# Optimization experiments

Hardware: AMD Instinct MI355X
Metric: run time of the kernel (lower is better)

Reference implementation:

```python
import jax, jax.numpy as jnp
import numpy as np

E, U, D, R = 200000, 50000, 128, 32
N2, N1, NU = 100000, 80000, 20000  # hop-2 frontier, hop-1 frontier, unreachable; N1+N2+NU == E
M1, M0 = 1600000, 800000


def setup_inputs() -> dict:
    key = jax.random.key(0)
    ks = jax.random.split(key, 16)
    inp = {
        'ent_emb': jax.random.normal(ks[0], (E, D), jnp.float32) * 0.1,
        'user_emb': jax.random.normal(ks[1], (U, D), jnp.float32) * 0.1,
        'rel_emb': jax.random.normal(ks[2], (R, D), jnp.float32) * 0.1,
        'W_self': jax.random.normal(ks[3], (D, D), jnp.float32) / np.sqrt(D),
        'W_nei': jax.random.normal(ks[4], (D, D), jnp.float32) / np.sqrt(D),
        'b': jnp.zeros((D,), jnp.float32),
        'final_indices': jax.random.randint(ks[5], (N2,), 0, E, jnp.int32),
        'ent_now1': jax.random.randint(ks[6], (N1,), 0, E, jnp.int32),
        'e1_src': jax.random.randint(ks[7], (M1,), 0, N2, jnp.int32),
        'e1_dst': jax.random.randint(ks[8], (M1,), 0, N1, jnp.int32),
        'e1_rel': jax.random.randint(ks[9], (M1,), 0, R, jnp.int32),
        'e0_src': jax.random.randint(ks[10], (M0,), 0, N1, jnp.int32),
        'e0_dst': jax.random.randint(ks[11], (M0,), 0, U, jnp.int32),
        'e0_rel': jax.random.randint(ks[12], (M0,), 0, R, jnp.int32),
        'unreach_idx': jax.random.randint(ks[13], (NU,), 0, E, jnp.int32),
        'order': jax.random.permutation(ks[14], E).astype(jnp.int32),
    }
    return inp


def _rgcn_layer(x, tail, src, dst, rel, W_self, W_nei, b, rel_emb, n_out, activate):
    # self transform: [N, D]
    out = x @ W_self + b
    if tail is not None:
        # gather neighbor reps + relation modulation: [M, D]
        msg = tail[src] * rel_emb[rel]
        agg = jax.ops.segment_sum(msg, dst, num_segments=n_out)
        deg = jax.ops.segment_sum(jnp.ones_like(dst, dtype=x.dtype), dst, num_segments=n_out)
        agg = agg / jnp.clip(deg, 1.0)[:, None]
        out = out + agg @ W_nei
    return jnp.tanh(out) if activate else out


def reference(ent_emb, user_emb, rel_emb, W_self, W_nei, b,
              final_indices, ent_now1, e1_src, e1_dst, e1_rel,
              e0_src, e0_dst, e0_rel, unreach_idx, order):
    # hop 2: raw gathered entity embeddings (deepest frontier)
    h2 = ent_emb[final_indices]                                            # [N2, D]
    # hop 1: RGCN over kg edges from hop-2 frontier
    h1 = _rgcn_layer(ent_emb[ent_now1], h2, e1_src, e1_dst, e1_rel,
                     W_self, W_nei, b, rel_emb, N1, activate=True)          # [N1, D]
    # hop 0: user representations, no activation (activate=False in source)
    user_rep = _rgcn_layer(user_emb, h1, e0_src, e0_dst, e0_rel,
                           W_self, W_nei, b, rel_emb, U, activate=False)    # [U, D]
    # unreachable entities: self-only transform (tail_rep=None)
    unreachable = _rgcn_layer(ent_emb[unreach_idx], None, None, None, None,
                              W_self, W_nei, b, rel_emb, NU, activate=True)  # [NU, D]
    # concat hop reps in forward hop order, then reindex-scatter by entity order
    ent_user_all = jnp.concatenate([h1, h2, unreachable], axis=0)[order]    # [E, D]
    return jnp.concatenate([user_rep, ent_user_all], axis=0)               # [U+E, D]
```

## Files before the change

### kernel.cpp

```cpp
#include <hip/hip_runtime.h>

#define E_  200000
#define U_  50000
#define D_  128
#define R_  32
#define N2_ 100000
#define N1_ 80000
#define NU_ 20000
#define M1_ 1600000
#define M0_ 800000

__device__ __forceinline__ float4 ld4(const float* p) {
    return *reinterpret_cast<const float4*>(p);
}
__device__ __forceinline__ void st4(float* p, float4 v) {
    *reinterpret_cast<float4*>(p) = v;
}

__device__ __forceinline__ float fast_tanh(float x) {
    float e = __expf(2.0f * x);
    return 1.0f - 2.0f / (e + 1.0f);
}

__global__ __launch_bounds__(256) void gather_rows_k(
    const float* __restrict__ src, const int* __restrict__ idx,
    float* __restrict__ out, int n)
{
    long long gid = (long long)blockIdx.x * blockDim.x + threadIdx.x;
    int i = (int)(gid >> 5);
    int l = (int)(gid & 31);
    if (i >= n) return;
    int s = idx[i];
    st4(out + (long long)i * 128 + l * 4, ld4(src + (long long)s * 128 + l * 4));
}

__global__ __launch_bounds__(256) void hist_k(
    const int* __restrict__ dst, int* __restrict__ cnt, int M)
{
    int i = blockIdx.x * blockDim.x + threadIdx.x;
    if (i < M) atomicAdd(&cnt[dst[i]], 1);
}

__global__ __launch_bounds__(1024) void scan_k(
    int* __restrict__ cur, int* __restrict__ off, int N)
{
    __shared__ int ls[1024];
    const int t = threadIdx.x;
    const int chunk = (N + 1023) >> 10;
    const int s = t * chunk;
    const int e = min(s + chunk, N);
    int sum = 0;
    for (int i = s; i < e; ++i) sum += cur[i];
    ls[t] = sum;
    __syncthreads();
    #pragma unroll
    for (int d = 1; d < 1024; d <<= 1) {
        int v = (t >= d) ? ls[t - d] : 0;
        __syncthreads();
        ls[t] += v;
        __syncthreads();
    }
    int run = (t == 0) ? 0 : ls[t - 1];
    for (int i = s; i < e; ++i) {
        int c = cur[i];
        off[i] = run;
        cur[i] = run;
        run += c;
    }
    if (t == 1023) off[N] = ls[1023];
}

__global__ __launch_bounds__(256) void fill_k(
    const int* __restrict__ src, const int* __restrict__ dst,
    const int* __restrict__ rel, int* __restrict__ cur,
    int* __restrict__ sorted, int M)
{
    int i = blockIdx.x * blockDim.x + threadIdx.x;
    if (i >= M) return;
    int p = atomicAdd(&cur[dst[i]], 1);
    sorted[p] = src[i] | (rel[i] << 20);
}

__global__ __launch_bounds__(256) void seg_reduce_k(
    const float* __restrict__ tail, const float* __restrict__ rel_emb,
    const int* __restrict__ off, const int* __restrict__ sorted,
    float* __restrict__ aggout, int N)
{
    long long gid = (long long)blockIdx.x * blockDim.x + threadIdx.x;
    int row = (int)(gid >> 5);
    int l = (int)(gid & 31) * 4;
    if (row >= N) return;
    int s = off[row], e = off[row + 1];
    float4 acc = make_float4(0.f, 0.f, 0.f, 0.f);
    int j = s;
    for (; j + 1 < e; j += 2) {
        int p0 = sorted[j], p1 = sorted[j + 1];
        float4 t0 = ld4(tail + (long long)(p0 & 0xFFFFF) * 128 + l);
        float4 r0 = ld4(rel_emb + (long long)(p0 >> 20) * 128 + l);
        float4 t1 = ld4(tail + (long long)(p1 & 0xFFFFF) * 128 + l);
        float4 r1 = ld4(rel_emb + (long long)(p1 >> 20) * 128 + l);
        acc.x = fmaf(t0.x, r0.x, acc.x); acc.y = fmaf(t0.y, r0.y, acc.y);
        acc.z = fmaf(t0.z, r0.z, acc.z); acc.w = fmaf(t0.w, r0.w, acc.w);
        acc.x = fmaf(t1.x, r1.x, acc.x); acc.y = fmaf(t1.y, r1.y, acc.y);
        acc.z = fmaf(t1.z, r1.z, acc.z); acc.w = fmaf(t1.w, r1.w, acc.w);
    }
    if (j < e) {
        int p0 = sorted[j];
        float4 t0 = ld4(tail + (long long)(p0 & 0xFFFFF) * 128 + l);
        float4 r0 = ld4(rel_emb + (long long)(p0 >> 20) * 128 + l);
        acc.x = fmaf(t0.x, r0.x, acc.x); acc.y = fmaf(t0.y, r0.y, acc.y);
        acc.z = fmaf(t0.z, r0.z, acc.z); acc.w = fmaf(t0.w, r0.w, acc.w);
    }
    float sc = 1.0f / (float)max(e - s, 1);
    acc.x *= sc; acc.y *= sc; acc.z *= sc; acc.w *= sc;
    st4(aggout + (long long)row * 128 + l, acc);
}

template<bool GATHER, bool ACCUM, bool BIAS, bool ACT>
__global__ __launch_bounds__(256) void gemm_rows_k(
    const float* __restrict__ X, const int* __restrict__ idx,
    const float* __restrict__ W, const float* __restrict__ bias,
    float* __restrict__ Out, int N)
{
    __shared__ float XsT[32][128];
    __shared__ float Ws [32][128];
    const int tid = threadIdx.x;
    const int rowbase = blockIdx.x * 128;
    const int rg = tid >> 4;
    const int cg = tid & 15;
    const int r0 = rg * 8;
    const int c0 = cg * 8;

    float acc[8][8];
    if (BIAS) {
        #pragma unroll
        for (int j = 0; j < 8; ++j) {
            float bv = bias[c0 + j];
            #pragma unroll
            for (int i = 0; i < 8; ++i) acc[i][j] = bv;
        }
    } else {
        #pragma unroll
        for (int i = 0; i < 8; ++i)
            #pragma unroll
            for (int j = 0; j < 8; ++j) acc[i][j] = 0.0f;
    }

    const int srow = tid >> 3;
    const int skq  = (tid & 7) * 4;
    const int sswz = (tid & 7) << 2;
    const int wkk  = tid >> 5;
    const int wcc  = (tid & 31) * 4;

    for (int k0 = 0; k0 < 128; k0 += 32) {
        __syncthreads();
        #pragma unroll
        for (int p = 0; p < 4; ++p) {
            int row = p * 32 + srow;
            int grow = rowbase + row;
            int cl = grow < N ? grow : (N - 1);
            const float* xr;
            if (GATHER) xr = X + (long long)idx[cl] * 128;
            else        xr = X + (long long)cl * 128;
            float4 v = ld4(xr + k0 + skq);
            int rs = row ^ sswz;
            XsT[skq + 0][rs] = v.x;
            XsT[skq + 1][rs] = v.y;
            XsT[skq + 2][rs] = v.z;
            XsT[skq + 3][rs] = v.w;
        }
        #pragma unroll
        for (int p = 0; p < 4; ++p) {
            int k = p * 8 + wkk;
            st4(&Ws[k][wcc], ld4(W + (long long)(k0 + k) * 128 + wcc));
        }
        __syncthreads();
        #pragma unroll
        for (int k = 0; k < 32; ++k) {
            int A0 = (((r0 >> 2) ^ ((k >> 2) & 7)) << 2);
            float4 x0 = ld4(&XsT[k][A0]);
            float4 x1 = ld4(&XsT[k][A0 ^ 4]);
            float4 w0 = ld4(&Ws[k][c0]);
            float4 w1 = ld4(&Ws[k][c0 + 4]);
            float xs[8] = {x0.x, x0.y, x0.z, x0.w, x1.x, x1.y, x1.z, x1.w};
            float ws[8] = {w0.x, w0.y, w0.z, w0.w, w1.x, w1.y, w1.z, w1.w};
            #pragma unroll
            for (int i = 0; i < 8; ++i)
                #pragma unroll
                for (int j = 0; j < 8; ++j)
                    acc[i][j] = fmaf(xs[i], ws[j], acc[i][j]);
        }
    }

    #pragma unroll
    for (int i = 0; i < 8; ++i) {
        int row = rowbase + r0 + i;
        if (row >= N) continue;
        float* op = Out + (long long)row * 128 + c0;
        float vals[8];
        #pragma unroll
        for (int j = 0; j < 8; ++j) vals[j] = acc[i][j];
        if (ACCUM) {
            float4 o0 = ld4(op), o1 = ld4(op + 4);
            vals[0] += o0.x; vals[1] += o0.y; vals[2] += o0.z; vals[3] += o0.w;
            vals[4] += o1.x; vals[5] += o1.y; vals[6] += o1.z; vals[7] += o1.w;
        }
        if (ACT) {
            #pragma unroll
            for (int j = 0; j < 8; ++j) vals[j] = fast_tanh(vals[j]);
        }
        st4(op,     make_float4(vals[0], vals[1], vals[2], vals[3]));
        st4(op + 4, make_float4(vals[4], vals[5], vals[6], vals[7]));
    }
}

extern "C" void kernel_launch(void* const* d_in, const int* in_sizes, int n_in,
                              void* d_out, int out_size, void* d_ws, size_t ws_size,
                              hipStream_t stream)
{
    const float* ent_emb  = (const float*)d_in[0];
    const float* user_emb = (const float*)d_in[1];
    const float* rel_emb  = (const float*)d_in[2];
    const float* W_self   = (const float*)d_in[3];
    const float* W_nei    = (const float*)d_in[4];
    const float* bvec     = (const float*)d_in[5];
    const int* final_indices = (const int*)d_in[6];
    const int* ent_now1   = (const int*)d_in[7];
    const int* e1_src     = (const int*)d_in[8];
    const int* e1_dst     = (const int*)d_in[9];
    const int* e1_rel     = (const int*)d_in[10];
    const int* e0_src     = (const int*)d_in[11];
    const int* e0_dst     = (const int*)d_in[12];
    const int* e0_rel     = (const int*)d_in[13];
    const int* unreach_idx = (const int*)d_in[14];
    const int* order      = (const int*)d_in[15];

    float* out = (float*)d_out;
    float* ws  = (float*)d_ws;

    float* concat = ws;
    float* agg1 = concat + (size_t)E_ * 128;
    float* agg0 = agg1 + (size_t)N1_ * 128;
    int* cur1 = (int*)(agg0 + (size_t)U_ * 128);
    int* cur0 = cur1 + N1_;
    int* off1 = cur0 + U_;
    int* off0 = off1 + (N1_ + 1);
    int* sorted1 = off0 + (U_ + 1);
    int* sorted0 = sorted1 + M1_;

    float* h1   = concat;
    float* h2   = concat + (size_t)N1_ * 128;
    float* unre = concat + (size_t)(N1_ + N2_) * 128;

    hipMemsetAsync(cur1, 0, (size_t)(N1_ + U_) * sizeof(int), stream);

    gather_rows_k<<<(N2_ * 32 + 255) / 256, 256, 0, stream>>>(
        ent_emb, final_indices, h2, N2_);

    hist_k<<<(M1_ + 255) / 256, 256, 0, stream>>>(e1_dst, cur1, M1_);
    scan_k<<<1, 1024, 0, stream>>>(cur1, off1, N1_);
    fill_k<<<(M1_ + 255) / 256, 256, 0, stream>>>(
        e1_src, e1_dst, e1_rel, cur1, sorted1, M1_);
    seg_reduce_k<<<(N1_ * 32 + 255) / 256, 256, 0, stream>>>(
        h2, rel_emb, off1, sorted1, agg1, N1_);

    gemm_rows_k<true,  false, true,  false><<<(N1_ + 127) / 128, 256, 0, stream>>>(
        ent_emb, ent_now1, W_self, bvec, h1, N1_);
    gemm_rows_k<false, true,  false, true ><<<(N1_ + 127) / 128, 256, 0, stream>>>(
        agg1, nullptr, W_nei, nullptr, h1, N1_);

    hist_k<<<(M0_ + 255) / 256, 256, 0, stream>>>(e0_dst, cur0, M0_);
    scan_k<<<1, 1024, 0, stream>>>(cur0, off0, U_);
    fill_k<<<(M0_ + 255) / 256, 256, 0, stream>>>(
        e0_src, e0_dst, e0_rel, cur0, sorted0, M0_);
    seg_reduce_k<<<(U_ * 32 + 255) / 256, 256, 0, stream>>>(
        h1, rel_emb, off0, sorted0, agg0, U_);

    gemm_rows_k<false, false, true,  false><<<(U_ + 127) / 128, 256, 0, stream>>>(
        user_emb, nullptr, W_self, bvec, out, U_);
    gemm_rows_k<false, true,  false, false><<<(U_ + 127) / 128, 256, 0, stream>>>(
        agg0, nullptr, W_nei, nullptr, out, U_);

    gemm_rows_k<true,  false, true,  true ><<<(NU_ + 127) / 128, 256, 0, stream>>>(
        ent_emb, unreach_idx, W_self, bvec, unre, NU_);

    gather_rows_k<<<(E_ * 32 + 255) / 256, 256, 0, stream>>>(
        concat, order, out + (size_t)U_ * 128, E_);
}
```

Baseline: 1.136 ms.

## Parallelize degree prefix scan and fuse self/neighbor GEMMs into one kernel

The single-block serial scan over per-destination counts becomes a three-kernel multi-block scan: block partial sums, a scan over the partials, then per-block apply. The paired self-transform and neighbor-transform GEMMs (run as a write followed by an accumulate pass) are merged into one kernel that stages both inputs and both weight tiles and accumulates into a single register tile. This avoids re-reading and re-writing the output between passes. It doubles shared memory per block (64KB), which may cut occupancy.

```diff
diff --git a/kernel.cpp b/kernel.cpp
--- a/kernel.cpp
+++ b/kernel.cpp
@@ -41,33 +41,83 @@
     if (i < M) atomicAdd(&cnt[dst[i]], 1);
 }
 
-__global__ __launch_bounds__(1024) void scan_k(
-    int* __restrict__ cur, int* __restrict__ off, int N)
-{
-    __shared__ int ls[1024];
+__global__ __launch_bounds__(256) void partial_sums_k(
+    const int* __restrict__ cnt, int* __restrict__ bsum, int N)
+{
+    __shared__ int sm[256];
     const int t = threadIdx.x;
-    const int chunk = (N + 1023) >> 10;
-    const int s = t * chunk;
-    const int e = min(s + chunk, N);
+    const int base = blockIdx.x * 1024;
     int sum = 0;
-    for (int i = s; i < e; ++i) sum += cur[i];
-    ls[t] = sum;
+    #pragma unroll
+    for (int i = 0; i < 4; ++i) {
+        int g = base + t + i * 256;
+        if (g < N) sum += cnt[g];
+    }
+    sm[t] = sum;
     __syncthreads();
     #pragma unroll
-    for (int d = 1; d < 1024; d <<= 1) {
-        int v = (t >= d) ? ls[t - d] : 0;
-        __syncthreads();
-        ls[t] += v;
-        __syncthreads();
-    }
-    int run = (t == 0) ? 0 : ls[t - 1];
-    for (int i = s; i < e; ++i) {
-        int c = cur[i];
-        off[i] = run;
-        cur[i] = run;
-        run += c;
-    }
-    if (t == 1023) off[N] = ls[1023];
+    for (int s = 128; s > 0; s >>= 1) {
+        if (t < s) sm[t] += sm[t + s];
+        __syncthreads();
+    }
+    if (t == 0) bsum[blockIdx.x] = sm[0];
+}
+
+__global__ __launch_bounds__(256) void scan_partials_k(
+    int* __restrict__ bsum, int NB, int* __restrict__ off, int N)
+{
+    __shared__ int ls[256];
+    const int t = threadIdx.x;
+    int v = (t < NB) ? bsum[t] : 0;
+    ls[t] = v;
+    __syncthreads();
+    #pragma unroll
+    for (int d = 1; d < 256; d <<= 1) {
+        int u = (t >= d) ? ls[t - d] : 0;
+        __syncthreads();
+        ls[t] += u;
+        __syncthreads();
+    }
+    if (t < NB) bsum[t] = ls[t] - v;
+    if (t == 255) off[N] = ls[255];
+}
+
+__global__ __launch_bounds__(256) void scan_apply_k(
+    const int* __restrict__ cnt, const int* __restrict__ bsum,
+    int* __restrict__ off, int* __restrict__ cur, int N)
+{
+    __shared__ int buf[1024];
+    __shared__ int ts[256];
+    const int t = threadIdx.x;
+    const int base = blockIdx.x * 1024;
+    #pragma unroll
+    for (int i = 0; i < 4; ++i) {
+        int g = base + t + i * 256;
+        buf[t + i * 256] = (g < N) ? cnt[g] : 0;
+    }
+    __syncthreads();
+    const int a = buf[t * 4], b = buf[t * 4 + 1], c = buf[t * 4 + 2], d = buf[t * 4 + 3];
+    const int s = a + b + c + d;
+    ts[t] = s;
+    __syncthreads();
+    #pragma unroll
+    for (int dd = 1; dd < 256; dd <<= 1) {
+        int u = (t >= dd) ? ts[t - dd] : 0;
+        __syncthreads();
+        ts[t] += u;
+        __syncthreads();
+    }
+    const int pre = bsum[blockIdx.x] + ts[t] - s;
+    const int o0 = pre, o1 = pre + a, o2 = o1 + b, o3 = o2 + c;
+    const int g0 = base + t * 4;
+    if (g0 + 3 < N) {
+        *reinterpret_cast<int4*>(off + g0) = make_int4(o0, o1, o2, o3);
+        *reinterpret_cast<int4*>(cur + g0) = make_int4(o0, o1, o2, o3);
+    } else {
+        if (g0     < N) { off[g0]     = o0; cur[g0]     = o0; }
+        if (g0 + 1 < N) { off[g0 + 1] = o1; cur[g0 + 1] = o1; }
+        if (g0 + 2 < N) { off[g0 + 2] = o2; cur[g0 + 2] = o2; }
+    }
 }
 
 __global__ __launch_bounds__(256) void fill_k(
@@ -126,10 +176,8 @@
     __shared__ float Ws [32][128];
     const int tid = threadIdx.x;
     const int rowbase = blockIdx.x * 128;
-    const int rg = tid >> 4;
-    const int cg = tid & 15;
-    const int r0 = rg * 8;
-    const int c0 = cg * 8;
+    const int r0 = (tid >> 4) * 8;
+    const int c0 = (tid & 15) * 8;
 
     float acc[8][8];
     if (BIAS) {
@@ -159,9 +207,8 @@
             int row = p * 32 + srow;
             int grow = rowbase + row;
             int cl = grow < N ? grow : (N - 1);
-            const float* xr;
-            if (GATHER) xr = X + (long long)idx[cl] * 128;
-            else        xr = X + (long long)cl * 128;
+            const float* xr = GATHER ? X + (long long)idx[cl] * 128
+                                     : X + (long long)cl * 128;
             float4 v = ld4(xr + k0 + skq);
             int rs = row ^ sswz;
             XsT[skq + 0][rs] = v.x;
@@ -205,6 +252,103 @@
             vals[0] += o0.x; vals[1] += o0.y; vals[2] += o0.z; vals[3] += o0.w;
             vals[4] += o1.x; vals[5] += o1.y; vals[6] += o1.z; vals[7] += o1.w;
         }
+        if (ACT) {
+            #pragma unroll
+            for (int j = 0; j < 8; ++j) vals[j] = fast_tanh(vals[j]);
+        }
+        st4(op,     make_float4(vals[0], vals[1], vals[2], vals[3]));
+        st4(op + 4, make_float4(vals[4], vals[5], vals[6], vals[7]));
+    }
+}
+
+template<bool GATHER1, bool ACT>
+__global__ __launch_bounds__(256) void gemm_fused_k(
+    const float* __restrict__ X1, const int* __restrict__ idx,
+    const float* __restrict__ X2,
+    const float* __restrict__ W1, const float* __restrict__ W2,
+    const float* __restrict__ bias, float* __restrict__ Out, int N)
+{
+    __shared__ float X1sT[32][128];
+    __shared__ float X2sT[32][128];
+    __shared__ float W1s [32][128];
+    __shared__ float W2s [32][128];
+    const int tid = threadIdx.x;
+    const int rowbase = blockIdx.x * 128;
+    const int r0 = (tid >> 4) * 8;
+    const int c0 = (tid & 15) * 8;
+
+    float acc[8][8];
+    #pragma unroll
+    for (int j = 0; j < 8; ++j) {
+        float bv = bias[c0 + j];
+        #pragma unroll
+        for (int i = 0; i < 8; ++i) acc[i][j] = bv;
+    }
+
+    const int srow = tid >> 3;
+    const int skq  = (tid & 7) * 4;
+    const int sswz = (tid & 7) << 2;
+    const int wkk  = tid >> 5;
+    const int wcc  = (tid & 31) * 4;
+
+    for (int k0 = 0; k0 < 128; k0 += 32) {
+        __syncthreads();
+        #pragma unroll
+        for (int p = 0; p < 4; ++p) {
+            int row = p * 32 + srow;
+            int grow = rowbase + row;
+            int cl = grow < N ? grow : (N - 1);
+            const float* x1r = GATHER1 ? X1 + (long long)idx[cl] * 128
+                                       : X1 + (long long)cl * 128;
+            const float* x2r = X2 + (long long)cl * 128;
+            float4 v1 = ld4(x1r + k0 + skq);
+            float4 v2 = ld4(x2r + k0 + skq);
+            int rs = row ^ sswz;
+            X1sT[skq + 0][rs] = v1.x; X1sT[skq + 1][rs] = v1.y;
+            X1sT[skq + 2][rs] = v1.z; X1sT[skq + 3][rs] = v1.w;
+            X2sT[skq + 0][rs] = v2.x; X2sT[skq + 1][rs] = v2.y;
+            X2sT[skq + 2][rs] = v2.z; X2sT[skq + 3][rs] = v2.w;
+        }
+        #pragma unroll
+        for (int p = 0; p < 4; ++p) {
+            int k = p * 8 + wkk;
+            st4(&W1s[k][wcc], ld4(W1 + (long long)(k0 + k) * 128 + wcc));
+            st4(&W2s[k][wcc], ld4(W2 + (long long)(k0 + k) * 128 + wcc));
+        }
+        __syncthreads();
+        #pragma unroll
+        for (int k = 0; k < 32; ++k) {
+            int A0 = (((r0 >> 2) ^ ((k >> 2) & 7)) << 2);
+            float4 a0 = ld4(&X1sT[k][A0]);
+            float4 a1 = ld4(&X1sT[k][A0 ^ 4]);
+            float4 b0 = ld4(&X2sT[k][A0]);
+            float4 b1 = ld4(&X2sT[k][A0 ^ 4]);
+            float4 u0 = ld4(&W1s[k][c0]);
+            float4 u1 = ld4(&W1s[k][c0 + 4]);
+            float4 v0 = ld4(&W2s[k][c0]);
+            float4 v1 = ld4(&W2s[k][c0 + 4]);
+            float x1s[8] = {a0.x, a0.y, a0.z, a0.w, a1.x, a1.y, a1.z, a1.w};
+            float x2s[8] = {b0.x, b0.y, b0.z, b0.w, b1.x, b1.y, b1.z, b1.w};
+            float w1s[8] = {u0.x, u0.y, u0.z, u0.w, u1.x, u1.y, u1.z, u1.w};
+            float w2s[8] = {v0.x, v0.y, v0.z, v0.w, v1.x, v1.y, v1.z, v1.w};
+            #pragma unroll
+            for (int i = 0; i < 8; ++i)
+                #pragma unroll
+                for (int j = 0; j < 8; ++j) {
+                    acc[i][j] = fmaf(x1s[i], w1s[j], acc[i][j]);
+                    acc[i][j] = fmaf(x2s[i], w2s[j], acc[i][j]);
+                }
+        }
+    }
+
+    #pragma unroll
+    for (int i = 0; i < 8; ++i) {
+        int row = rowbase + r0 + i;
+        if (row >= N) continue;
+        float* op = Out + (long long)row * 128 + c0;
+        float vals[8];
+        #pragma unroll
+        for (int j = 0; j < 8; ++j) vals[j] = acc[i][j];
         if (ACT) {
             #pragma unroll
             for (int j = 0; j < 8; ++j) vals[j] = fast_tanh(vals[j]);
@@ -244,44 +388,49 @@
     int* cur1 = (int*)(agg0 + (size_t)U_ * 128);
     int* cur0 = cur1 + N1_;
     int* off1 = cur0 + U_;
-    int* off0 = off1 + (N1_ + 1);
-    int* sorted1 = off0 + (U_ + 1);
+    int* off0 = off1 + (N1_ + 4);
+    int* bsum1 = off0 + (U_ + 4);
+    int* bsum0 = bsum1 + 256;
+    int* sorted1 = bsum0 + 256;
     int* sorted0 = sorted1 + M1_;
 
     float* h1   = concat;
     float* h2   = concat + (size_t)N1_ * 128;
     float* unre = concat + (size_t)(N1_ + N2_) * 128;
 
+    const int NB1 = (N1_ + 1023) / 1024;
+    const int NB0 = (U_  + 1023) / 1024;
+
     hipMemsetAsync(cur1, 0, (size_t)(N1_ + U_) * sizeof(int), stream);
 
     gather_rows_k<<<(N2_ * 32 + 255) / 256, 256, 0, stream>>>(
         ent_emb, final_indices, h2, N2_);
 
     hist_k<<<(M1_ + 255) / 256, 256, 0, stream>>>(e1_dst, cur1, M1_);
-    scan_k<<<1, 1024, 0, stream>>>(cur1, off1, N1_);
+    partial_sums_k<<<NB1, 256, 0, stream>>>(cur1, bsum1, N1_);
+    scan_partials_k<<<1, 256, 0, stream>>>(bsum1, NB1, off1, N1_);
+    scan_apply_k<<<NB1, 256, 0, stream>>>(cur1, bsum1, off1, cur1, N1_);
     fill_k<<<(M1_ + 255) / 256, 256, 0, stream>>>(
         e1_src, e1_dst, e1_rel, cur1, sorted1, M1_);
     seg_reduce_k<<<(N1_ * 32 + 255) / 256, 256, 0, stream>>>(
         h2, rel_emb, off1, sorted1, agg1, N1_);
 
-    gemm_rows_k<true,  false, true,  false><<<(N1_ + 127) / 128, 256, 0, stream>>>(
-        ent_emb, ent_now1, W_self, bvec, h1, N1_);
-    gemm_rows_k<false, true,  false, true ><<<(N1_ + 127) / 128, 256, 0, stream>>>(
-        agg1, nullptr, W_nei, nullptr, h1, N1_);
+    gemm_fused_k<true, true><<<(N1_ + 127) / 128, 256, 0, stream>>>(
+        ent_emb, ent_now1, agg1, W_self, W_nei, bvec, h1, N1_);
 
     hist_k<<<(M0_ + 255) / 256, 256, 0, stream>>>(e0_dst, cur0, M0_);
-    scan_k<<<1, 1024, 0, stream>>>(cur0, off0, U_);
+    partial_sums_k<<<NB0, 256, 0, stream>>>(cur0, bsum0, U_);
+    scan_partials_k<<<1, 256, 0, stream>>>(bsum0, NB0, off0, U_);
+    scan_apply_k<<<NB0, 256, 0, stream>>>(cur0, bsum0, off0, cur0, U_);
     fill_k<<<(M0_ + 255) / 256, 256, 0, stream>>>(
         e0_src, e0_dst, e0_rel, cur0, sorted0, M0_);
     seg_reduce_k<<<(U_ * 32 + 255) / 256, 256, 0, stream>>>(
         h1, rel_emb, off0, sorted0, agg0, U_);
 
-    gemm_rows_k<false, false, true,  false><<<(U_ + 127) / 128, 256, 0, stream>>>(
-        user_emb, nullptr, W_self, bvec, out, U_);
-    gemm_rows_k<false, true,  false, false><<<(U_ + 127) / 128, 256, 0, stream>>>(
-        agg0, nullptr, W_nei, nullptr, out, U_);
-
-    gemm_rows_k<true,  false, true,  true ><<<(NU_ + 127) / 128, 256, 0, stream>>>(
+    gemm_fused_k<false, false><<<(U_ + 127) / 128, 256, 0, stream>>>(
+        user_emb, nullptr, agg0, W_self, W_nei, bvec, out, U_);
+
+    gemm_rows_k<true, false, true, true><<<(NU_ + 127) / 128, 256, 0, stream>>>(
         ent_emb, unreach_idx, W_self, bvec, unre, NU_);
 
     gather_rows_k<<<(E_ * 32 + 255) / 256, 256, 0, stream>>>(
```

After: 912.2 us. -19.7%, faster.
